# Optimization experiments

Hardware: AMD Instinct MI355X
Metric: run time of the kernel (lower is better)

## Reference

```python
import jax, jax.numpy as jnp
import numpy as np

IN_DIM = 512
OUT_DIM = 512
GRID_SIZE = 7
K = 4
N_KNOTS = GRID_SIZE + 2 * K + 1  # 16
N_BASIS = GRID_SIZE + K          # 11
BATCH = 16384


def b_splines(x, grid, k):
    # x: (B, in_dim), grid: (in_dim, N_KNOTS)
    x = x[..., None]  # (B, in, 1)
    value = ((x >= grid[:, :-1]) & (x < grid[:, 1:])).astype(x.dtype)  # (B, in, N_KNOTS-1)
    for p in range(1, k + 1):
        diff_left = grid[:, p:-1] - grid[:, :-(p + 1)]
        diff_right = grid[:, p + 1:] - grid[:, 1:-p]
        safe_dl = jnp.where(diff_left != 0, diff_left, 1.0)
        safe_dr = jnp.where(diff_right != 0, diff_right, 1.0)
        ratio_left = jnp.where(diff_left != 0, (x - grid[:, :-(p + 1)]) / safe_dl, 0.0)
        ratio_right = jnp.where(diff_right != 0, (grid[:, p + 1:] - x) / safe_dr, 0.0)
        value = (ratio_left * value[..., :-1] + ratio_right * value[..., 1:]) / (
            ratio_left + ratio_right + 1e-8)
    return value  # (B, in, N_BASIS)


def setup_inputs() -> dict:
    key = jax.random.key(0)
    k1, k2, k3, k4 = jax.random.split(key, 4)
    x = jax.random.uniform(k1, (BATCH, IN_DIM), dtype=jnp.float32)
    grid = jnp.tile(jnp.linspace(-1.0, 1.0, N_KNOTS, dtype=jnp.float32)[None, :], (IN_DIM, 1))
    coeff = jax.random.normal(k2, (OUT_DIM, IN_DIM, N_BASIS), dtype=jnp.float32) * 0.05
    scale_base = 1.0 / IN_DIM ** 0.5 + (
        jax.random.normal(k3, (OUT_DIM, IN_DIM), dtype=jnp.float32) * 2.0 - 1.0) * 0.05
    scale_spline = jnp.ones((OUT_DIM, IN_DIM), dtype=jnp.float32)
    bias = jnp.zeros((1, OUT_DIM), dtype=jnp.float32)
    return {"x": x, "grid": grid, "coeff": coeff, "scale_base": scale_base,
            "scale_spline": scale_spline, "bias": bias}


def reference(x, grid, coeff, scale_base, scale_spline, bias):
    shape = x.shape[:-1]
    x2 = x.reshape(-1, IN_DIM)
    splines = b_splines(x2, grid, K)                         # (B, in, N_BASIS)
    base_act = x2 + jnp.sin(x2)                              # KolmogorovActivation
    y_b = jnp.einsum('bi,oi->bo', base_act, scale_base)
    y_spline = jnp.einsum('bik,oik->bo', splines, coeff * scale_spline[:, :, None])
    y = y_b + y_spline + bias
    return y.reshape(*shape, OUT_DIM)
```

## Files before the change

kernel.cpp:

```cpp
#include <hip/hip_runtime.h>
#include <hip/hip_bf16.h>
#include <stdint.h>

#define IN_DIM  512
#define OUT_DIM 512
#define BATCH   16384
#define KPF     12
#define BM      128
#define BN      256
#define BK      96
#define KCH     64
#define TSTR    104
#define TILE_E  (BN * TSTR)

typedef __bf16 bf16;
typedef __bf16 bf16x8 __attribute__((ext_vector_type(8)));
typedef float  f32x4  __attribute__((ext_vector_type(4)));

__device__ __forceinline__ void gl2lds16(const void* g, void* l) {
    __builtin_amdgcn_global_load_lds((__attribute__((address_space(1))) uint32_t*)g,
                                     (__attribute__((address_space(3))) uint32_t*)l,
                                     16, 0, 0);
}
__device__ __forceinline__ uint bfbits(float v) {
    union { bf16 h; ushort u; } c; c.h = (bf16)v; return (uint)c.u;
}
__device__ __forceinline__ uint pk2(float lo, float hi) {
    return bfbits(lo) | (bfbits(hi) << 16);
}

__global__ void pack_w(const float* __restrict__ coeff,
                       const float* __restrict__ sbase,
                       const float* __restrict__ sspl,
                       bf16* __restrict__ W2) {
    __shared__ float cs[11 * 256];
    const int tid  = threadIdx.x;
    const int base = blockIdx.x * 256;
    const float* src = coeff + (size_t)base * 11;
#pragma unroll
    for (int j = 0; j < 11; ++j) cs[j * 256 + tid] = src[j * 256 + tid];
    __syncthreads();
    const int gid = base + tid;
    const int o = gid >> 9, i = gid & 511;
    const float s = sspl[gid];
    const float* cp = cs + tid * 11;
    union { bf16 hh[12]; uint2 uu[3]; } pk;
#pragma unroll
    for (int k = 0; k < 11; ++k) pk.hh[k] = (bf16)(cp[k] * s);
    pk.hh[11] = (bf16)sbase[gid];
    const int g = o >> 8, r = o & 255, kc = i >> 3, ic = i & 7;
    uint2* dst = (uint2*)(W2 + ((size_t)(g * 64 + kc) * 256 + r) * TSTR + ic * 12);
    dst[0] = pk.uu[0]; dst[1] = pk.uu[1]; dst[2] = pk.uu[2];
}

__global__ void __launch_bounds__(512, 2) kan_gemm(
    const float* __restrict__ xg,
    const float* __restrict__ gridp,
    const float* __restrict__ bias,
    const bf16*  __restrict__ W2,
    float* __restrict__ out)
{
    __shared__ bf16 Abuf[2 * BM * TSTR];
    __shared__ bf16 Bbuf[2 * BN * TSTR];

    const int tid  = threadIdx.x;
    const int lane = tid & 63;
    const int wave = tid >> 6;
    const int g  = blockIdx.x;
    const int n0 = g * BN;
    const int m0 = blockIdx.y * BM;

    const float g0    = gridp[0];
    const float inv_h = 1.0f / (gridp[1] - gridp[0]);

    const bf16* Wg = W2 + (size_t)g * KCH * TILE_E;
    const int nIss = (wave < 4) ? 7 : 6;

    const int row_e = tid & 127;
    const int fpair = tid >> 7;
    const float* xrow = xg + (size_t)(m0 + row_e) * IN_DIM + fpair * 2;

    const int wm = wave & 1, wn = wave >> 1;
    const int lr = lane & 15, lq = lane >> 4;

    f32x4 acc[4][4];
#pragma unroll
    for (int mt = 0; mt < 4; ++mt)
#pragma unroll
        for (int nt = 0; nt < 4; ++nt) { f32x4 z = {0.f, 0.f, 0.f, 0.f}; acc[mt][nt] = z; }

    auto evalOne = [&](float xv, uint* De) {
        float f  = __builtin_fmaf(xv, inv_h, -g0 * inv_h);
        f = fminf(fmaxf(f, 7.0f), 14.9999f);
        float fj = floorf(f);
        int   j0 = (int)fj;
        float t  = f - fj;
        float t1 = t + 1.0f, t2 = t + 2.0f, t3 = t + 3.0f;
        float s1 = 1.0f - t, s2 = 2.0f - t, s3 = 3.0f - t, s4 = 4.0f - t;
        float a0 = 0.5f * t, a1 = 0.5f * s1;
        const float i3 = (1.0f / 3.0f);
        float b0 = t  * a0 * i3;
        float b1 = (t1 * a1 + s2 * a0) * i3;
        float b2 = s1 * a1 * i3;
        float c0 = t  * b0 * 0.25f;
        float c1 = (t1 * b1 + s3 * b0) * 0.25f;
        float c2 = (t2 * b2 + s2 * b1) * 0.25f;
        float c3 = s1 * b2 * 0.25f;
        float w0 = t  * c0 * 0.2f;
        float w1 = (t1 * c1 + s4 * c0) * 0.2f;
        float w2 = (t2 * c2 + s3 * c1) * 0.2f;
        float w3 = (t3 * c3 + s2 * c2) * 0.2f;
        float w4 = s1 * c3 * 0.2f;
        const int q0 = j0 - 4;
        const int rr = q0 & 1;
        const int d  = q0 >> 1;
        uint P0 = pk2(w4, w3), P1 = pk2(w2, w1), P2 = bfbits(w0);
        uint A0 = rr ? (P0 << 16)                : P0;
        uint A1 = rr ? ((P0 >> 16) | (P1 << 16)) : P1;
        uint A2 = rr ? ((P1 >> 16) | (P2 << 16)) : P2;
        De[0] = 0u;
        De[1] = (d == 1) ? A0 : 0u;
        De[2] = (d == 2) ? A0 : ((d == 1) ? A1 : 0u);
        De[3] = (d == 3) ? A0 : ((d == 2) ? A1 : ((d == 1) ? A2 : 0u));
        De[4] = (d == 4) ? A0 : ((d == 3) ? A1 : ((d == 2) ? A2 : 0u));
        uint D5 = (d == 5) ? A0 : ((d == 4) ? A1 : ((d == 3) ? A2 : 0u));
        De[5] = (D5 & 0xFFFFu) | (bfbits(xv + __sinf(xv)) << 16);
    };
    auto evalPair = [&](float2 xc, bf16* Adst) {
        uint D[12];
        evalOne(xc.x, D);
        evalOne(xc.y, D + 6);
        uint4* awr = (uint4*)(Adst + row_e * TSTR + fpair * 24);
        awr[0] = make_uint4(D[0], D[1], D[2],  D[3]);
        awr[1] = make_uint4(D[4], D[5], D[6],  D[7]);
        awr[2] = make_uint4(D[8], D[9], D[10], D[11]);
    };
    auto dmaB = [&](int kc, bf16* Bdst) {
        const bf16* wsc = Wg + (size_t)kc * TILE_E;
#pragma unroll
        for (int j = 0; j < 7; ++j) {
            if (j < nIss) {
                int iss = wave + 8 * j;
                gl2lds16(wsc + iss * 512 + lane * 8, Bdst + iss * 512);
            }
        }
    };

    dmaB(0, Bbuf);
    float2 xb0 = *(const float2*)(xrow);
    float2 xb1 = *(const float2*)(xrow + 8);
    evalPair(xb0, Abuf);
    xb0 = *(const float2*)(xrow + 16);
    __syncthreads();

    for (int kc = 0; kc < KCH; ++kc) {
        const int p = kc & 1;
        if (kc < KCH - 1) {
            dmaB(kc + 1, Bbuf + (p ^ 1) * BN * TSTR);
            float2 xc = (kc & 1) ? xb0 : xb1;
            evalPair(xc, Abuf + (p ^ 1) * BM * TSTR);
            float2 xn = *(const float2*)(xrow + (((kc + 3) & (KCH - 1)) << 3));
            if (kc & 1) xb0 = xn; else xb1 = xn;
        }

        const bf16* Ap = Abuf + p * BM * TSTR;
        const bf16* Bp = Bbuf + p * BN * TSTR;
#pragma unroll
        for (int s = 0; s < 3; ++s) {
            bf16x8 af[4], bfr[4];
#pragma unroll
            for (int mt = 0; mt < 4; ++mt)
                af[mt] = *(const bf16x8*)&Ap[(wm * 64 + mt * 16 + lr) * TSTR + s * 32 + lq * 8];
#pragma unroll
            for (int nt = 0; nt < 4; ++nt)
                bfr[nt] = *(const bf16x8*)&Bp[(wn * 64 + nt * 16 + lr) * TSTR + s * 32 + lq * 8];
#pragma unroll
            for (int mt = 0; mt < 4; ++mt)
#pragma unroll
                for (int nt = 0; nt < 4; ++nt)
                    acc[mt][nt] = __builtin_amdgcn_mfma_f32_16x16x32_bf16(
                        af[mt], bfr[nt], acc[mt][nt], 0, 0, 0);
        }
        __syncthreads();
    }

#pragma unroll
    for (int nt = 0; nt < 4; ++nt) {
        const int gcol = n0 + wn * 64 + nt * 16 + lr;
        const float bv = bias[gcol];
#pragma unroll
        for (int mt = 0; mt < 4; ++mt) {
#pragma unroll
            for (int i = 0; i < 4; ++i) {
                const int grow = m0 + wm * 64 + mt * 16 + lq * 4 + i;
                out[(size_t)grow * OUT_DIM + gcol] = acc[mt][nt][i] + bv;
            }
        }
    }
}

extern "C" void kernel_launch(void* const* d_in, const int* in_sizes, int n_in,
                              void* d_out, int out_size, void* d_ws, size_t ws_size,
                              hipStream_t stream) {
    const float* x     = (const float*)d_in[0];
    const float* gridv = (const float*)d_in[1];
    const float* coeff = (const float*)d_in[2];
    const float* sbase = (const float*)d_in[3];
    const float* sspl  = (const float*)d_in[4];
    const float* bias  = (const float*)d_in[5];
    float* out = (float*)d_out;
    bf16*  W2  = (bf16*)d_ws;

    pack_w<<<dim3((OUT_DIM * IN_DIM) / 256), 256, 0, stream>>>(coeff, sbase, sspl, W2);
    kan_gemm<<<dim3(OUT_DIM / BN, BATCH / BM), 512, 0, stream>>>(x, gridv, bias, W2, out);
}
```

Before: 207.7 us.

## Load B fragments directly from global into registers, drop LDS staging

The GEMM kernel no longer copies weight tiles into shared memory. Each wave now loads its B fragments straight from global memory into registers every k-chunk, which frees half the LDS and removes the DMA issue logic. The pack kernel is rewritten so each thread packs a full 96-element row with a dense 96 stride, using only 128 blocks. The B loads are no longer prefetched a stage ahead, so global latency may sit in front of the MFMAs. Register pressure also rises, and the pack kernel has far fewer threads.

```diff
diff --git a/kernel.cpp b/kernel.cpp
--- a/kernel.cpp
+++ b/kernel.cpp
@@ -5,23 +5,17 @@
 #define IN_DIM  512
 #define OUT_DIM 512
 #define BATCH   16384
-#define KPF     12
 #define BM      128
 #define BN      256
 #define BK      96
 #define KCH     64
 #define TSTR    104
-#define TILE_E  (BN * TSTR)
+#define TILE    (256 * 96)
 
 typedef __bf16 bf16;
 typedef __bf16 bf16x8 __attribute__((ext_vector_type(8)));
 typedef float  f32x4  __attribute__((ext_vector_type(4)));
 
-__device__ __forceinline__ void gl2lds16(const void* g, void* l) {
-    __builtin_amdgcn_global_load_lds((__attribute__((address_space(1))) uint32_t*)g,
-                                     (__attribute__((address_space(3))) uint32_t*)l,
-                                     16, 0, 0);
-}
 __device__ __forceinline__ uint bfbits(float v) {
     union { bf16 h; ushort u; } c; c.h = (bf16)v; return (uint)c.u;
 }
@@ -33,24 +27,29 @@
                        const float* __restrict__ sbase,
                        const float* __restrict__ sspl,
                        bf16* __restrict__ W2) {
-    __shared__ float cs[11 * 256];
-    const int tid  = threadIdx.x;
-    const int base = blockIdx.x * 256;
-    const float* src = coeff + (size_t)base * 11;
-#pragma unroll
-    for (int j = 0; j < 11; ++j) cs[j * 256 + tid] = src[j * 256 + tid];
-    __syncthreads();
-    const int gid = base + tid;
-    const int o = gid >> 9, i = gid & 511;
-    const float s = sspl[gid];
-    const float* cp = cs + tid * 11;
-    union { bf16 hh[12]; uint2 uu[3]; } pk;
-#pragma unroll
-    for (int k = 0; k < 11; ++k) pk.hh[k] = (bf16)(cp[k] * s);
-    pk.hh[11] = (bf16)sbase[gid];
-    const int g = o >> 8, r = o & 255, kc = i >> 3, ic = i & 7;
-    uint2* dst = (uint2*)(W2 + ((size_t)(g * 64 + kc) * 256 + r) * TSTR + ic * 12);
-    dst[0] = pk.uu[0]; dst[1] = pk.uu[1]; dst[2] = pk.uu[2];
+    const int b  = blockIdx.x;
+    const int g  = b >> 6, kc = b & 63;
+    const int t  = threadIdx.x;
+    const int o  = g * 256 + t;
+    const float* cp = coeff + (size_t)o * (512 * 11) + kc * 88;
+    float c[88];
+#pragma unroll
+    for (int j = 0; j < 22; ++j) *(float4*)(c + 4 * j) = *(const float4*)(cp + 4 * j);
+    float ss[8], bb[8];
+    *(float4*)(ss)     = *(const float4*)(sspl  + (size_t)o * 512 + kc * 8);
+    *(float4*)(ss + 4) = *(const float4*)(sspl  + (size_t)o * 512 + kc * 8 + 4);
+    *(float4*)(bb)     = *(const float4*)(sbase + (size_t)o * 512 + kc * 8);
+    *(float4*)(bb + 4) = *(const float4*)(sbase + (size_t)o * 512 + kc * 8 + 4);
+    union { bf16 hh[96]; uint4 uu[12]; } pk;
+#pragma unroll
+    for (int ic = 0; ic < 8; ++ic) {
+#pragma unroll
+        for (int k = 0; k < 11; ++k) pk.hh[ic * 12 + k] = (bf16)(c[ic * 11 + k] * ss[ic]);
+        pk.hh[ic * 12 + 11] = (bf16)bb[ic];
+    }
+    uint4* dst = (uint4*)(W2 + ((size_t)b * 256 + t) * 96);
+#pragma unroll
+    for (int j = 0; j < 12; ++j) dst[j] = pk.uu[j];
 }
 
 __global__ void __launch_bounds__(512, 2) kan_gemm(
@@ -61,7 +60,6 @@
     float* __restrict__ out)
 {
     __shared__ bf16 Abuf[2 * BM * TSTR];
-    __shared__ bf16 Bbuf[2 * BN * TSTR];
 
     const int tid  = threadIdx.x;
     const int lane = tid & 63;
@@ -73,15 +71,14 @@
     const float g0    = gridp[0];
     const float inv_h = 1.0f / (gridp[1] - gridp[0]);
 
-    const bf16* Wg = W2 + (size_t)g * KCH * TILE_E;
-    const int nIss = (wave < 4) ? 7 : 6;
+    const int wm = wave & 1, wn = wave >> 1;
+    const int lr = lane & 15, lq = lane >> 4;
+
+    const bf16* Bw = W2 + (size_t)g * KCH * TILE + (wn * 64 + lr) * 96 + lq * 8;
 
     const int row_e = tid & 127;
     const int fpair = tid >> 7;
     const float* xrow = xg + (size_t)(m0 + row_e) * IN_DIM + fpair * 2;
-
-    const int wm = wave & 1, wn = wave >> 1;
-    const int lr = lane & 15, lq = lane >> 4;
 
     f32x4 acc[4][4];
 #pragma unroll
@@ -135,18 +132,7 @@
         awr[1] = make_uint4(D[4], D[5], D[6],  D[7]);
         awr[2] = make_uint4(D[8], D[9], D[10], D[11]);
     };
-    auto dmaB = [&](int kc, bf16* Bdst) {
-        const bf16* wsc = Wg + (size_t)kc * TILE_E;
-#pragma unroll
-        for (int j = 0; j < 7; ++j) {
-            if (j < nIss) {
-                int iss = wave + 8 * j;
-                gl2lds16(wsc + iss * 512 + lane * 8, Bdst + iss * 512);
-            }
-        }
-    };
-
-    dmaB(0, Bbuf);
+
     float2 xb0 = *(const float2*)(xrow);
     float2 xb1 = *(const float2*)(xrow + 8);
     evalPair(xb0, Abuf);
@@ -155,8 +141,16 @@
 
     for (int kc = 0; kc < KCH; ++kc) {
         const int p = kc & 1;
+
+        const bf16* Bk = Bw + (size_t)kc * TILE;
+        bf16x8 bq[12];
+#pragma unroll
+        for (int s = 0; s < 3; ++s)
+#pragma unroll
+            for (int nt = 0; nt < 4; ++nt)
+                bq[s * 4 + nt] = *(const bf16x8*)(Bk + nt * (16 * 96) + s * 32);
+
         if (kc < KCH - 1) {
-            dmaB(kc + 1, Bbuf + (p ^ 1) * BN * TSTR);
             float2 xc = (kc & 1) ? xb0 : xb1;
             evalPair(xc, Abuf + (p ^ 1) * BM * TSTR);
             float2 xn = *(const float2*)(xrow + (((kc + 3) & (KCH - 1)) << 3));
@@ -164,22 +158,18 @@
         }
 
         const bf16* Ap = Abuf + p * BM * TSTR;
-        const bf16* Bp = Bbuf + p * BN * TSTR;
 #pragma unroll
         for (int s = 0; s < 3; ++s) {
-            bf16x8 af[4], bfr[4];
+            bf16x8 af[4];
 #pragma unroll
             for (int mt = 0; mt < 4; ++mt)
                 af[mt] = *(const bf16x8*)&Ap[(wm * 64 + mt * 16 + lr) * TSTR + s * 32 + lq * 8];
 #pragma unroll
-            for (int nt = 0; nt < 4; ++nt)
-                bfr[nt] = *(const bf16x8*)&Bp[(wn * 64 + nt * 16 + lr) * TSTR + s * 32 + lq * 8];
-#pragma unroll
             for (int mt = 0; mt < 4; ++mt)
 #pragma unroll
                 for (int nt = 0; nt < 4; ++nt)
                     acc[mt][nt] = __builtin_amdgcn_mfma_f32_16x16x32_bf16(
-                        af[mt], bfr[nt], acc[mt][nt], 0, 0, 0);
+                        af[mt], bq[s * 4 + nt], acc[mt][nt], 0, 0, 0);
         }
         __syncthreads();
     }
@@ -211,6 +201,6 @@
     float* out = (float*)d_out;
     bf16*  W2  = (bf16*)d_ws;
 
-    pack_w<<<dim3((OUT_DIM * IN_DIM) / 256), 256, 0, stream>>>(coeff, sbase, sspl, W2);
+    pack_w<<<dim3(128), 256, 0, stream>>>(coeff, sbase, sspl, W2);
     kan_gemm<<<dim3(OUT_DIM / BN, BATCH / BM), 512, 0, stream>>>(x, gridv, bias, W2, out);
 }
```

Result: slower. 275.4 us (+32.6%).
